# Performance work log

Hardware: AMD Instinct MI355X
Metric: run time of the kernel (lower is better)

Reference implementation:

```python
import jax, jax.numpy as jnp
import numpy as np

HIDDEN = 1024
NUM_HEADS = 16
HEAD_DIM = HIDDEN // NUM_HEADS  # 64
ROPE_DIM = HEAD_DIM // 2        # 32 (per-axis rotary dim)
EPS = 1e-6


def _make_rope_tables(dim, grid_h, grid_w, theta=10000.0):
    # pt_seq_len == ft_seq_len, so t_h = arange(H), t_w = arange(W)
    freqs = 1.0 / theta ** (np.arange(0, dim, 2, dtype=np.float32)[: dim // 2] / dim)  # [dim//2]
    fh = np.repeat(np.outer(np.arange(grid_h, dtype=np.float32), freqs), 2, axis=-1)  # [H, dim]
    fw = np.repeat(np.outer(np.arange(grid_w, dtype=np.float32), freqs), 2, axis=-1)  # [W, dim]
    fh = np.broadcast_to(fh[:, None, :], (grid_h, grid_w, dim))
    fw = np.broadcast_to(fw[None, :, :], (grid_h, grid_w, dim))
    f2d = np.concatenate([fh, fw], axis=-1).reshape(grid_h * grid_w, 2 * dim)  # [HW, 2*dim]
    return jnp.asarray(np.cos(f2d)), jnp.asarray(np.sin(f2d))


def _rms_norm(x, w, eps=EPS):
    var = jnp.mean(jnp.square(x), axis=-1, keepdims=True)
    return x * jax.lax.rsqrt(var + eps) * w


def _rotate_half(x):
    x1 = x[..., 0::2]
    x2 = x[..., 1::2]
    return jnp.stack([-x2, x1], axis=-1).reshape(x.shape)


def _apply_rope(x, cos, sin):
    # x: [B, H, S, D]; cos/sin: [S, D]
    return x * cos + _rotate_half(x) * sin


def setup_inputs() -> dict:
    key = jax.random.key(0)
    ks = jax.random.split(key, 12)
    B, IMG_H, IMG_W, CND_H, CND_W = 2, 64, 64, 32, 32
    img_len, cnd_len = IMG_H * IMG_W, CND_H * CND_W
    xav = (6.0 / (HIDDEN + HIDDEN)) ** 0.5
    inp = {
        'image_tokens': jax.random.normal(ks[0], (B, img_len, HIDDEN), jnp.float32),
        'condition_tokens': jax.random.normal(ks[1], (B, cnd_len, HIDDEN), jnp.float32),
        'q_norm_w': jnp.ones((HIDDEN,), jnp.float32),
        'kv_norm_w': jnp.ones((HIDDEN,), jnp.float32),
        'q_head_norm_w': jnp.ones((HEAD_DIM,), jnp.float32),
        'k_head_norm_w': jnp.ones((HEAD_DIM,), jnp.float32),
        'q_w': jax.random.uniform(ks[2], (HIDDEN, HIDDEN), jnp.float32, -xav, xav),
        'q_b': jnp.zeros((HIDDEN,), jnp.float32),
        'k_w': jax.random.uniform(ks[3], (HIDDEN, HIDDEN), jnp.float32, -xav, xav),
        'k_b': jnp.zeros((HIDDEN,), jnp.float32),
        'v_w': jax.random.uniform(ks[4], (HIDDEN, HIDDEN), jnp.float32, -xav, xav),
        'v_b': jnp.zeros((HIDDEN,), jnp.float32),
        'o_w': jax.random.uniform(ks[5], (HIDDEN, HIDDEN), jnp.float32, -xav, xav),
        'o_b': jnp.zeros((HIDDEN,), jnp.float32),
        'alpha': jnp.full((1,), 0.5, jnp.float32),  # nonzero so backward exercises the attn path
    }
    ic, isn = _make_rope_tables(ROPE_DIM, IMG_H, IMG_W)
    cc, cs = _make_rope_tables(ROPE_DIM, CND_H, CND_W)
    inp.update(image_cos=ic, image_sin=isn, cond_cos=cc, cond_sin=cs)
    return inp


def reference(image_tokens, condition_tokens, q_norm_w, kv_norm_w, q_head_norm_w,
              k_head_norm_w, q_w, q_b, k_w, k_b, v_w, v_b, o_w, o_b, alpha,
              image_cos, image_sin, cond_cos, cond_sin):
    B, Li, _ = image_tokens.shape
    Lc = condition_tokens.shape[1]
    qn = _rms_norm(image_tokens, q_norm_w)
    kvn = _rms_norm(condition_tokens, kv_norm_w)
    # projections (torch Linear: x @ W.T + b); weights here stored [out, in]
    q = (qn @ q_w.T + q_b).reshape(B, Li, NUM_HEADS, HEAD_DIM).transpose(0, 2, 1, 3)
    k = (kvn @ k_w.T + k_b).reshape(B, Lc, NUM_HEADS, HEAD_DIM).transpose(0, 2, 1, 3)
    v = (kvn @ v_w.T + v_b).reshape(B, Lc, NUM_HEADS, HEAD_DIM).transpose(0, 2, 1, 3)
    q = _rms_norm(q, q_head_norm_w)
    k = _rms_norm(k, k_head_norm_w)
    q = _apply_rope(q, image_cos, image_sin)
    k = _apply_rope(k, cond_cos, cond_sin)
    scale = 1.0 / jnp.sqrt(jnp.asarray(HEAD_DIM, q.dtype))
    scores = jnp.einsum('bhqd,bhkd->bhqk', q, k) * scale
    attn = jax.nn.softmax(scores, axis=-1)
    out = jnp.einsum('bhqk,bhkd->bhqd', attn, v)
    out = out.transpose(0, 2, 1, 3).reshape(B, Li, HIDDEN)
    update = out @ o_w.T + o_b
    return image_tokens + alpha.reshape(1, 1, 1) * update
```

## Files before the change

### kernel.cpp

```cpp
#include <hip/hip_runtime.h>

typedef __bf16 bf16x8 __attribute__((ext_vector_type(8)));
typedef __bf16 bf16x4 __attribute__((ext_vector_type(4)));
typedef float  f32x4  __attribute__((ext_vector_type(4)));
typedef float  f32x16 __attribute__((ext_vector_type(16)));
typedef unsigned u32x2 __attribute__((ext_vector_type(2)));

#define DEVINL __device__ __forceinline__

DEVINL void gload_lds16(const void* g, void* l) {
  __builtin_amdgcn_global_load_lds((const __attribute__((address_space(1))) void*)g,
                                   (__attribute__((address_space(3))) void*)l, 16, 0, 0);
}

DEVINL unsigned pkbf(float a, float b) {
  union { __bf16 h[2]; unsigned u; } c;
  c.h[0] = (__bf16)a; c.h[1] = (__bf16)b;
  return c.u;
}

DEVINL float fast_exp2(float x) {
#if __has_builtin(__builtin_amdgcn_exp2f)
  return __builtin_amdgcn_exp2f(x);
#else
  float r;
  asm volatile("v_exp_f32 %0, %1" : "=v"(r) : "v"(x));
  return r;
#endif
}

DEVINL float2 swap32(float x) {
  u32x2 r = __builtin_amdgcn_permlane32_swap(__float_as_uint(x), __float_as_uint(x), false, false);
  return make_float2(__uint_as_float(r.x), __uint_as_float(r.y));
}

__global__ __launch_bounds__(256) void rmsnorm2_kernel(
    const float* __restrict__ XA, const float* __restrict__ WA, __bf16* __restrict__ YA, int nA,
    const float* __restrict__ XB, const float* __restrict__ WB, __bf16* __restrict__ YB) {
  int rb = blockIdx.x, tid = threadIdx.x;
  const float* X; const float* W; __bf16* Y; int row;
  if (rb < nA) { X = XA; W = WA; Y = YA; row = rb; }
  else { X = XB; W = WB; Y = YB; row = rb - nA; }
  const float4* xr = (const float4*)(X + (size_t)row * 1024);
  float4 v = xr[tid];
  float ss = v.x * v.x + v.y * v.y + v.z * v.z + v.w * v.w;
#pragma unroll
  for (int m = 1; m < 64; m <<= 1) ss += __shfl_xor(ss, m);
  __shared__ float part[4];
  if ((tid & 63) == 0) part[tid >> 6] = ss;
  __syncthreads();
  float tot = part[0] + part[1] + part[2] + part[3];
  float rn = rsqrtf(tot * (1.0f / 1024.0f) + 1e-6f);
  float4 wv = ((const float4*)W)[tid];
  bf16x4 y;
  y[0] = (__bf16)(v.x * rn * wv.x);
  y[1] = (__bf16)(v.y * rn * wv.y);
  y[2] = (__bf16)(v.z * rn * wv.z);
  y[3] = (__bf16)(v.w * rn * wv.w);
  *(bf16x4*)(Y + (size_t)row * 1024 + tid * 4) = y;
}

__global__ __launch_bounds__(256) void cast_w_kernel(
    const float* __restrict__ a, const float* __restrict__ b,
    const float* __restrict__ c, const float* __restrict__ d,
    __bf16* __restrict__ oa, __bf16* __restrict__ ob,
    __bf16* __restrict__ oc, __bf16* __restrict__ od) {
  int gid = blockIdx.x * 256 + threadIdx.x;
  int which = gid >> 17;
  size_t off = (size_t)(gid & 131071) * 8;
  const float* s = (which == 0) ? a : (which == 1) ? b : (which == 2) ? c : d;
  __bf16* o = (which == 0) ? oa : (which == 1) ? ob : (which == 2) ? oc : od;
  float4 v0 = *(const float4*)(s + off), v1 = *(const float4*)(s + off + 4);
  bf16x8 y;
  y[0] = (__bf16)v0.x; y[1] = (__bf16)v0.y; y[2] = (__bf16)v0.z; y[3] = (__bf16)v0.w;
  y[4] = (__bf16)v1.x; y[5] = (__bf16)v1.y; y[6] = (__bf16)v1.z; y[7] = (__bf16)v1.w;
  *(bf16x8*)(o + off) = y;
}

template <int EPI>
__global__ __launch_bounds__(256) void gemm_bt_kernel(
    const __bf16* __restrict__ A, const __bf16* __restrict__ Bw,
    const float* __restrict__ bias, void* __restrict__ Cout,
    const float* __restrict__ resid, const float* __restrict__ alphap,
    const float* __restrict__ bias2, void* __restrict__ Cout2) {
  __shared__ __attribute__((aligned(16))) __bf16 As[128 * 32];
  __shared__ __attribute__((aligned(16))) __bf16 Bs[128 * 32];
  int tid = threadIdx.x, lane = tid & 63, w = tid >> 6, wr = w >> 1, wc = w & 1;
  int m0 = blockIdx.x * 128, n0 = blockIdx.y * 128;
  f32x4 z4 = {0.f, 0.f, 0.f, 0.f};
  f32x4 acc[4][4];
#pragma unroll
  for (int i = 0; i < 4; i++)
#pragma unroll
    for (int j = 0; j < 4; j++) acc[i][j] = z4;

  for (int k0 = 0; k0 < 1024; k0 += 32) {
#pragma unroll
    for (int i = 0; i < 2; i++) {
      int chunk = i * 256 + tid;
      int row = chunk >> 2, cc = chunk & 3;
      gload_lds16(A + (size_t)(m0 + row) * 1024 + k0 + cc * 8, (char*)As + i * 4096 + w * 1024);
      gload_lds16(Bw + (size_t)(n0 + row) * 1024 + k0 + cc * 8, (char*)Bs + i * 4096 + w * 1024);
    }
    __syncthreads();
    bf16x8 af[4], bfr[4];
#pragma unroll
    for (int m = 0; m < 4; m++) {
      int r = wr * 64 + m * 16 + (lane & 15);
      af[m] = *(const bf16x8*)((const char*)As + r * 64 + ((lane >> 4) << 4));
    }
#pragma unroll
    for (int n = 0; n < 4; n++) {
      int r = wc * 64 + n * 16 + (lane & 15);
      bfr[n] = *(const bf16x8*)((const char*)Bs + r * 64 + ((lane >> 4) << 4));
    }
#pragma unroll
    for (int m = 0; m < 4; m++)
#pragma unroll
      for (int n = 0; n < 4; n++)
        acc[m][n] = __builtin_amdgcn_mfma_f32_16x16x32_bf16(af[m], bfr[n], acc[m][n], 0, 0, 0);
    __syncthreads();
  }

  const float* biasU = bias;
  void* coutU = Cout;
  int nloc = n0;
  if (EPI == 2 && n0 >= 1024) { biasU = bias2; coutU = Cout2; nloc = n0 - 1024; }
  float aval = (EPI == 1) ? alphap[0] : 0.f;
#pragma unroll
  for (int m = 0; m < 4; m++)
#pragma unroll
    for (int n = 0; n < 4; n++) {
      int col = nloc + wc * 64 + n * 16 + (lane & 15);
      float bv = biasU[col];
#pragma unroll
      for (int r = 0; r < 4; r++) {
        int row = m0 + wr * 64 + m * 16 + ((lane >> 4) << 2) + r;
        size_t idx = ((size_t)row << 10) + col;
        float v = acc[m][n][r] + bv;
        if (EPI == 1)
          ((float*)coutU)[idx] = resid[idx] + aval * v;
        else
          ((__bf16*)coutU)[idx] = (__bf16)v;
      }
    }
}

__global__ __launch_bounds__(256) void headnorm_rope_kernel(
    const __bf16* __restrict__ X, const float* __restrict__ HW,
    const float* __restrict__ COS, const float* __restrict__ SIN,
    __bf16* __restrict__ Y, int log2L, float scale) {
  int tid = threadIdx.x;
  int inst = blockIdx.x * 32 + (tid >> 3);
  int sub = tid & 7;
  int token = inst >> 4, h = inst & 15;
  int L = 1 << log2L;
  int b = token >> log2L, pos = token & (L - 1);
  const __bf16* xp = X + ((size_t)token << 10) + h * 64 + sub * 8;
  bf16x8 xv = *(const bf16x8*)xp;
  float xf[8];
#pragma unroll
  for (int i = 0; i < 8; i++) xf[i] = (float)xv[i];
  float ss = 0.f;
#pragma unroll
  for (int i = 0; i < 8; i++) ss += xf[i] * xf[i];
  ss += __shfl_xor(ss, 1);
  ss += __shfl_xor(ss, 2);
  ss += __shfl_xor(ss, 4);
  float rn = rsqrtf(ss * (1.0f / 64.0f) + 1e-6f);
  const float* hwp = HW + sub * 8;
  const float* cp = COS + ((size_t)pos << 6) + sub * 8;
  const float* sp = SIN + ((size_t)pos << 6) + sub * 8;
  float xn[8], o[8];
#pragma unroll
  for (int i = 0; i < 8; i++) xn[i] = xf[i] * rn * hwp[i];
#pragma unroll
  for (int i = 0; i < 8; i += 2) {
    float c0 = cp[i], c1 = cp[i + 1], s0 = sp[i], s1 = sp[i + 1];
    o[i] = (xn[i] * c0 - xn[i + 1] * s0) * scale;
    o[i + 1] = (xn[i + 1] * c1 + xn[i] * s1) * scale;
  }
  bf16x8 yv;
#pragma unroll
  for (int i = 0; i < 8; i++) yv[i] = (__bf16)o[i];
  *(bf16x8*)(Y + (((size_t)((b << 4) + h) << log2L) + pos) * 64 + sub * 8) = yv;
}

__global__ __launch_bounds__(256) void v_transpose_kernel(
    const __bf16* __restrict__ V, __bf16* __restrict__ Vt) {
  int bx = blockIdx.x;
  int bh = bx >> 4;
  int j0 = (bx & 15) * 64;
  int b = bh >> 4, h = bh & 15;
  int tid = threadIdx.x;
#pragma unroll
  for (int it = 0; it < 2; ++it) {
    int c = it * 256 + tid;
    int jl = c >> 3, d0 = (c & 7) * 8;
    bf16x8 v = *(const bf16x8*)(V + (size_t)(b * 1024 + j0 + jl) * 1024 + h * 64 + d0);
#pragma unroll
    for (int i = 0; i < 8; i++)
      Vt[((size_t)bh * 64 + d0 + i) * 1024 + j0 + jl] = v[i];
  }
}

__global__ __launch_bounds__(256, 2) void attn_kernel(
    const __bf16* __restrict__ Qt, const float* __restrict__ QHW,
    const float* __restrict__ QCOS, const float* __restrict__ QSIN,
    const __bf16* __restrict__ Kr, const __bf16* __restrict__ Vtr,
    __bf16* __restrict__ AO) {
  int tid = threadIdx.x, lane = tid & 63, w = tid >> 6;
  int lq = lane & 31, hi = lane >> 5;
  int q0 = blockIdx.x * 256;
  int bh = blockIdx.y, b = bh >> 4, h = bh & 15;
  const float QSC = 0.125f * 1.44269504088896340736f;

  __shared__ __attribute__((aligned(16))) __bf16 Ks[2][4096];
  __shared__ __attribute__((aligned(16))) __bf16 Vs[2][4096];

  const __bf16* Kbh = Kr + ((size_t)bh << 16);
  const __bf16* Vbh = Vtr + ((size_t)bh << 16);

#pragma unroll
  for (int i = 0; i < 2; i++) {
    int s = 2 * w + i;
    int kt = s >> 2, ds = s & 3;
    gload_lds16(Kbh + (size_t)(kt * 32 + lq) * 64 + ds * 16 + hi * 8,
                (char*)Ks[0] + s * 1024);
    int f = s >> 1, dh = s & 1;
    gload_lds16(Vbh + (size_t)(dh * 32 + lq) * 1024 + f * 16 + hi * 8,
                (char*)Vs[0] + s * 1024);
  }

  bf16x8 qf[2][4];
#pragma unroll
  for (int qt = 0; qt < 2; qt++) {
    int pos = q0 + w * 64 + qt * 32 + lq;
    const __bf16* qp = Qt + ((size_t)(b * 4096 + pos) << 10) + h * 64 + hi * 8;
    float xf[4][8];
    float ss = 0.f;
#pragma unroll
    for (int ds = 0; ds < 4; ds++) {
      bf16x8 xv = *(const bf16x8*)(qp + ds * 16);
#pragma unroll
      for (int j = 0; j < 8; j++) { float f = (float)xv[j]; xf[ds][j] = f; ss += f * f; }
    }
    float2 sw = swap32(ss);
    float rn = rsqrtf((sw.x + sw.y) * (1.0f / 64.0f) + 1e-6f);
#pragma unroll
    for (int ds = 0; ds < 4; ds++) {
      int d0 = ds * 16 + hi * 8;
      const float* wp = QHW + d0;
      const float* cp = QCOS + ((size_t)pos << 6) + d0;
      const float* sp = QSIN + ((size_t)pos << 6) + d0;
      float4 wa = *(const float4*)wp, wb = *(const float4*)(wp + 4);
      float4 ca = *(const float4*)cp, cb = *(const float4*)(cp + 4);
      float4 sa = *(const float4*)sp, sb = *(const float4*)(sp + 4);
      float wv[8] = {wa.x, wa.y, wa.z, wa.w, wb.x, wb.y, wb.z, wb.w};
      float cv[8] = {ca.x, ca.y, ca.z, ca.w, cb.x, cb.y, cb.z, cb.w};
      float sv[8] = {sa.x, sa.y, sa.z, sa.w, sb.x, sb.y, sb.z, sb.w};
      float xn[8];
#pragma unroll
      for (int j = 0; j < 8; j++) xn[j] = xf[ds][j] * rn * wv[j];
      bf16x8 q8;
#pragma unroll
      for (int j = 0; j < 8; j += 2) {
        q8[j]     = (__bf16)((xn[j] * cv[j] - xn[j + 1] * sv[j]) * QSC);
        q8[j + 1] = (__bf16)((xn[j + 1] * cv[j + 1] + xn[j] * sv[j + 1]) * QSC);
      }
      qf[qt][ds] = q8;
    }
  }

  f32x16 Z16;
#pragma unroll
  for (int r = 0; r < 16; r++) Z16[r] = 0.f;

  f32x16 accO[2][2];
#pragma unroll
  for (int qt = 0; qt < 2; qt++)
#pragma unroll
    for (int dh = 0; dh < 2; dh++) accO[qt][dh] = Z16;
  float srun[2] = {0.f, 0.f};

  __syncthreads();

  int buf = 0;
  for (int t = 0; t < 16; t++) {
    if (t < 15) {
#pragma unroll
      for (int i = 0; i < 2; i++) {
        int s = 2 * w + i;
        int kt = s >> 2, ds = s & 3;
        gload_lds16(Kbh + (size_t)((t + 1) * 64 + kt * 32 + lq) * 64 + ds * 16 + hi * 8,
                    (char*)Ks[buf ^ 1] + s * 1024);
        int f = s >> 1, dh = s & 1;
        gload_lds16(Vbh + (size_t)(dh * 32 + lq) * 1024 + (t + 1) * 64 + f * 16 + hi * 8,
                    (char*)Vs[buf ^ 1] + s * 1024);
      }
    }
    const char* kbase = (const char*)Ks[buf];
    const char* vbase = (const char*)Vs[buf];
    int loff = lane * 16;

    bf16x8 kf[8], vf[8];
#pragma unroll
    for (int s = 0; s < 8; s++) kf[s] = *(const bf16x8*)(kbase + s * 1024 + loff);
#pragma unroll
    for (int s = 0; s < 8; s++) vf[s] = *(const bf16x8*)(vbase + s * 1024 + loff);

    f32x16 accS[2][2];
    __builtin_amdgcn_s_setprio(1);
#pragma unroll
    for (int qt = 0; qt < 2; qt++)
#pragma unroll
      for (int kt = 0; kt < 2; kt++) {
        accS[qt][kt] = __builtin_amdgcn_mfma_f32_32x32x16_bf16(kf[kt * 4], qf[qt][0], Z16, 0, 0, 0);
#pragma unroll
        for (int ds = 1; ds < 4; ds++)
          accS[qt][kt] = __builtin_amdgcn_mfma_f32_32x32x16_bf16(kf[kt * 4 + ds], qf[qt][ds], accS[qt][kt], 0, 0, 0);
      }
    __builtin_amdgcn_s_setprio(0);

    unsigned pa[2][4][4];
#pragma unroll
    for (int qt = 0; qt < 2; qt++) {
      float ssum = 0.f;
#pragma unroll
      for (int kt = 0; kt < 2; kt++)
#pragma unroll
        for (int r = 0; r < 16; r++) {
          float e = fast_exp2(accS[qt][kt][r]);
          accS[qt][kt][r] = e;
          ssum += e;
        }
      float2 sws = swap32(ssum);
      srun[qt] += sws.x + sws.y;
#pragma unroll
      for (int kt = 0; kt < 2; kt++)
#pragma unroll
        for (int s2 = 0; s2 < 2; s2++) {
          int f = kt * 2 + s2, rb = s2 * 8;
          unsigned u  = pkbf(accS[qt][kt][rb + 0], accS[qt][kt][rb + 1]);
          unsigned v2 = pkbf(accS[qt][kt][rb + 2], accS[qt][kt][rb + 3]);
          unsigned w2 = pkbf(accS[qt][kt][rb + 4], accS[qt][kt][rb + 5]);
          unsigned x2 = pkbf(accS[qt][kt][rb + 6], accS[qt][kt][rb + 7]);
          u32x2 r02 = __builtin_amdgcn_permlane32_swap(u, w2, false, false);
          u32x2 r13 = __builtin_amdgcn_permlane32_swap(v2, x2, false, false);
          pa[qt][f][0] = r02.x; pa[qt][f][1] = r13.x; pa[qt][f][2] = r02.y; pa[qt][f][3] = r13.y;
        }
    }

    __builtin_amdgcn_s_setprio(1);
#pragma unroll
    for (int f = 0; f < 4; f++)
#pragma unroll
      for (int qt = 0; qt < 2; qt++) {
        union { unsigned u[4]; bf16x8 v; } pf;
        pf.u[0] = pa[qt][f][0]; pf.u[1] = pa[qt][f][1];
        pf.u[2] = pa[qt][f][2]; pf.u[3] = pa[qt][f][3];
#pragma unroll
        for (int dh = 0; dh < 2; dh++)
          accO[qt][dh] = __builtin_amdgcn_mfma_f32_32x32x16_bf16(pf.v, vf[f * 2 + dh], accO[qt][dh], 0, 0, 0);
      }
    __builtin_amdgcn_s_setprio(0);
    __syncthreads();
    buf ^= 1;
  }

  __bf16* aobase = AO + (((size_t)b * 4096) << 10) + h * 64;
#pragma unroll
  for (int qt = 0; qt < 2; qt++) {
    float rinv = 1.0f / srun[qt];
    int ri = __float_as_int(rinv);
#pragma unroll
    for (int r = 0; r < 16; r++) {
      int cr = (r & 3) + ((r >> 2) << 3) + (hi << 2);
      float rv = __int_as_float(__builtin_amdgcn_ds_bpermute(cr << 2, ri));
      size_t rowoff = ((size_t)(q0 + w * 64 + qt * 32 + cr) << 10);
#pragma unroll
      for (int dh = 0; dh < 2; dh++)
        aobase[rowoff + dh * 32 + lq] = (__bf16)(accO[qt][dh][r] * rv);
    }
  }
}

extern "C" void kernel_launch(void* const* d_in, const int* in_sizes, int n_in,
                              void* d_out, int out_size, void* d_ws, size_t ws_size,
                              hipStream_t stream) {
  const float* img  = (const float*)d_in[0];
  const float* cnd  = (const float*)d_in[1];
  const float* qnw  = (const float*)d_in[2];
  const float* kvnw = (const float*)d_in[3];
  const float* qhw  = (const float*)d_in[4];
  const float* khw  = (const float*)d_in[5];
  const float* qw   = (const float*)d_in[6];
  const float* qb   = (const float*)d_in[7];
  const float* kw   = (const float*)d_in[8];
  const float* kb   = (const float*)d_in[9];
  const float* vw   = (const float*)d_in[10];
  const float* vb   = (const float*)d_in[11];
  const float* ow   = (const float*)d_in[12];
  const float* ob   = (const float*)d_in[13];
  const float* alpha= (const float*)d_in[14];
  const float* icos = (const float*)d_in[15];
  const float* isin = (const float*)d_in[16];
  const float* ccos = (const float*)d_in[17];
  const float* csin = (const float*)d_in[18];
  float* out = (float*)d_out;

  __bf16* p = (__bf16*)d_ws;
  __bf16* wqb = p; p += 1048576;
  __bf16* wkb = p; p += 1048576;
  __bf16* wvb = p; p += 1048576;
  __bf16* wob = p; p += 1048576;
  __bf16* qn  = p; p += 8388608;
  __bf16* kvn = p; p += 2097152;
  __bf16* Qt  = p; p += 8388608;
  __bf16* Kt  = p; p += 2097152;
  __bf16* Vt0 = p; p += 2097152;
  __bf16* Kr  = p; p += 2097152;
  __bf16* Vtr = p; p += 2097152;
  __bf16* AO  = qn;

  rmsnorm2_kernel<<<10240, 256, 0, stream>>>(img, qnw, qn, 8192, cnd, kvnw, kvn);
  cast_w_kernel<<<2048, 256, 0, stream>>>(qw, kw, vw, ow, wqb, wkb, wvb, wob);

  gemm_bt_kernel<0><<<dim3(64, 8), 256, 0, stream>>>(qn, wqb, qb, Qt, nullptr, nullptr, nullptr, nullptr);
  gemm_bt_kernel<2><<<dim3(16, 16), 256, 0, stream>>>(kvn, wkb, kb, Kt, nullptr, nullptr, vb, Vt0);

  headnorm_rope_kernel<<<1024, 256, 0, stream>>>(Kt, khw, ccos, csin, Kr, 10, 1.0f);
  v_transpose_kernel<<<512, 256, 0, stream>>>(Vt0, Vtr);

  attn_kernel<<<dim3(16, 32), 256, 0, stream>>>(Qt, qhw, icos, isin, Kr, Vtr, AO);

  gemm_bt_kernel<1><<<dim3(64, 8), 256, 0, stream>>>(AO, wob, ob, out, img, alpha, nullptr, nullptr);
}
```

Measured before the change: 162.1 us.

## Merge launches and triple-buffer attention K/V loads with remapped block order

```diff
diff --git a/kernel.cpp b/kernel.cpp
--- a/kernel.cpp
+++ b/kernel.cpp
@@ -34,55 +34,123 @@
   return make_float2(__uint_as_float(r.x), __uint_as_float(r.y));
 }
 
-__global__ __launch_bounds__(256) void rmsnorm2_kernel(
-    const float* __restrict__ XA, const float* __restrict__ WA, __bf16* __restrict__ YA, int nA,
-    const float* __restrict__ XB, const float* __restrict__ WB, __bf16* __restrict__ YB) {
+__global__ __launch_bounds__(256) void prep_kernel(
+    const float* __restrict__ XA, const float* __restrict__ WA, __bf16* __restrict__ YA,
+    const float* __restrict__ XB, const float* __restrict__ WB, __bf16* __restrict__ YB,
+    const float* __restrict__ wq, const float* __restrict__ wk,
+    const float* __restrict__ wv, const float* __restrict__ wo,
+    __bf16* __restrict__ oq, __bf16* __restrict__ ok,
+    __bf16* __restrict__ ov, __bf16* __restrict__ oo) {
   int rb = blockIdx.x, tid = threadIdx.x;
-  const float* X; const float* W; __bf16* Y; int row;
-  if (rb < nA) { X = XA; W = WA; Y = YA; row = rb; }
-  else { X = XB; W = WB; Y = YB; row = rb - nA; }
-  const float4* xr = (const float4*)(X + (size_t)row * 1024);
-  float4 v = xr[tid];
-  float ss = v.x * v.x + v.y * v.y + v.z * v.z + v.w * v.w;
-#pragma unroll
-  for (int m = 1; m < 64; m <<= 1) ss += __shfl_xor(ss, m);
-  __shared__ float part[4];
-  if ((tid & 63) == 0) part[tid >> 6] = ss;
-  __syncthreads();
-  float tot = part[0] + part[1] + part[2] + part[3];
-  float rn = rsqrtf(tot * (1.0f / 1024.0f) + 1e-6f);
-  float4 wv = ((const float4*)W)[tid];
-  bf16x4 y;
-  y[0] = (__bf16)(v.x * rn * wv.x);
-  y[1] = (__bf16)(v.y * rn * wv.y);
-  y[2] = (__bf16)(v.z * rn * wv.z);
-  y[3] = (__bf16)(v.w * rn * wv.w);
-  *(bf16x4*)(Y + (size_t)row * 1024 + tid * 4) = y;
-}
-
-__global__ __launch_bounds__(256) void cast_w_kernel(
-    const float* __restrict__ a, const float* __restrict__ b,
-    const float* __restrict__ c, const float* __restrict__ d,
-    __bf16* __restrict__ oa, __bf16* __restrict__ ob,
-    __bf16* __restrict__ oc, __bf16* __restrict__ od) {
-  int gid = blockIdx.x * 256 + threadIdx.x;
-  int which = gid >> 17;
-  size_t off = (size_t)(gid & 131071) * 8;
-  const float* s = (which == 0) ? a : (which == 1) ? b : (which == 2) ? c : d;
-  __bf16* o = (which == 0) ? oa : (which == 1) ? ob : (which == 2) ? oc : od;
-  float4 v0 = *(const float4*)(s + off), v1 = *(const float4*)(s + off + 4);
-  bf16x8 y;
-  y[0] = (__bf16)v0.x; y[1] = (__bf16)v0.y; y[2] = (__bf16)v0.z; y[3] = (__bf16)v0.w;
-  y[4] = (__bf16)v1.x; y[5] = (__bf16)v1.y; y[6] = (__bf16)v1.z; y[7] = (__bf16)v1.w;
-  *(bf16x8*)(o + off) = y;
-}
-
-template <int EPI>
-__global__ __launch_bounds__(256) void gemm_bt_kernel(
+  if (rb < 10240) {
+    const float* X; const float* W; __bf16* Y; int row;
+    if (rb < 8192) { X = XA; W = WA; Y = YA; row = rb; }
+    else { X = XB; W = WB; Y = YB; row = rb - 8192; }
+    const float4* xr = (const float4*)(X + (size_t)row * 1024);
+    float4 v = xr[tid];
+    float ss = v.x * v.x + v.y * v.y + v.z * v.z + v.w * v.w;
+#pragma unroll
+    for (int m = 1; m < 64; m <<= 1) ss += __shfl_xor(ss, m);
+    __shared__ float part[4];
+    if ((tid & 63) == 0) part[tid >> 6] = ss;
+    __syncthreads();
+    float tot = part[0] + part[1] + part[2] + part[3];
+    float rn = rsqrtf(tot * (1.0f / 1024.0f) + 1e-6f);
+    float4 wv4 = ((const float4*)W)[tid];
+    bf16x4 y;
+    y[0] = (__bf16)(v.x * rn * wv4.x);
+    y[1] = (__bf16)(v.y * rn * wv4.y);
+    y[2] = (__bf16)(v.z * rn * wv4.z);
+    y[3] = (__bf16)(v.w * rn * wv4.w);
+    *(bf16x4*)(Y + (size_t)row * 1024 + tid * 4) = y;
+  } else {
+    int gid = (rb - 10240) * 256 + tid;
+    int which = gid >> 17;
+    size_t off = (size_t)(gid & 131071) * 8;
+    const float* s = (which == 0) ? wq : (which == 1) ? wk : (which == 2) ? wv : wo;
+    __bf16* o = (which == 0) ? oq : (which == 1) ? ok : (which == 2) ? ov : oo;
+    float4 v0 = *(const float4*)(s + off), v1 = *(const float4*)(s + off + 4);
+    bf16x8 y;
+    y[0] = (__bf16)v0.x; y[1] = (__bf16)v0.y; y[2] = (__bf16)v0.z; y[3] = (__bf16)v0.w;
+    y[4] = (__bf16)v1.x; y[5] = (__bf16)v1.y; y[6] = (__bf16)v1.z; y[7] = (__bf16)v1.w;
+    *(bf16x8*)(o + off) = y;
+  }
+}
+
+__global__ __launch_bounds__(256) void qkv_gemm_kernel(
+    const __bf16* __restrict__ qn, const __bf16* __restrict__ kvn,
+    const __bf16* __restrict__ wq, const __bf16* __restrict__ wkv,
+    const float* __restrict__ qb, const float* __restrict__ kb, const float* __restrict__ vb,
+    __bf16* __restrict__ Qt, __bf16* __restrict__ Kt, __bf16* __restrict__ Vt0) {
+  __shared__ __attribute__((aligned(16))) __bf16 As[128 * 32];
+  __shared__ __attribute__((aligned(16))) __bf16 Bs[128 * 32];
+  int id = blockIdx.x;
+  const __bf16 *A, *Bw; const float* bias; __bf16* Cout;
+  int m0, n0, nloc;
+  if (id < 512) {
+    A = qn; Bw = wq; m0 = (id & 63) * 128; n0 = (id >> 6) * 128; nloc = n0;
+    bias = qb; Cout = Qt;
+  } else {
+    int i2 = id - 512;
+    A = kvn; Bw = wkv; m0 = (i2 & 15) * 128; n0 = (i2 >> 4) * 128;
+    if (n0 < 1024) { bias = kb; Cout = Kt; nloc = n0; }
+    else { bias = vb; Cout = Vt0; nloc = n0 - 1024; }
+  }
+  int tid = threadIdx.x, lane = tid & 63, w = tid >> 6, wr = w >> 1, wc = w & 1;
+  f32x4 z4 = {0.f, 0.f, 0.f, 0.f};
+  f32x4 acc[4][4];
+#pragma unroll
+  for (int i = 0; i < 4; i++)
+#pragma unroll
+    for (int j = 0; j < 4; j++) acc[i][j] = z4;
+
+  for (int k0 = 0; k0 < 1024; k0 += 32) {
+#pragma unroll
+    for (int i = 0; i < 2; i++) {
+      int chunk = i * 256 + tid;
+      int row = chunk >> 2, cc = chunk & 3;
+      gload_lds16(A + (size_t)(m0 + row) * 1024 + k0 + cc * 8, (char*)As + i * 4096 + w * 1024);
+      gload_lds16(Bw + (size_t)(n0 + row) * 1024 + k0 + cc * 8, (char*)Bs + i * 4096 + w * 1024);
+    }
+    __syncthreads();
+    bf16x8 af[4], bfr[4];
+#pragma unroll
+    for (int m = 0; m < 4; m++) {
+      int r = wr * 64 + m * 16 + (lane & 15);
+      af[m] = *(const bf16x8*)((const char*)As + r * 64 + ((lane >> 4) << 4));
+    }
+#pragma unroll
+    for (int n = 0; n < 4; n++) {
+      int r = wc * 64 + n * 16 + (lane & 15);
+      bfr[n] = *(const bf16x8*)((const char*)Bs + r * 64 + ((lane >> 4) << 4));
+    }
+#pragma unroll
+    for (int m = 0; m < 4; m++)
+#pragma unroll
+      for (int n = 0; n < 4; n++)
+        acc[m][n] = __builtin_amdgcn_mfma_f32_16x16x32_bf16(af[m], bfr[n], acc[m][n], 0, 0, 0);
+    __syncthreads();
+  }
+
+#pragma unroll
+  for (int m = 0; m < 4; m++)
+#pragma unroll
+    for (int n = 0; n < 4; n++) {
+      int col = nloc + wc * 64 + n * 16 + (lane & 15);
+      float bv = bias[col];
+#pragma unroll
+      for (int r = 0; r < 4; r++) {
+        int row = m0 + wr * 64 + m * 16 + ((lane >> 4) << 2) + r;
+        size_t idx = ((size_t)row << 10) + col;
+        Cout[idx] = (__bf16)(acc[m][n][r] + bv);
+      }
+    }
+}
+
+__global__ __launch_bounds__(256) void gemm_o_kernel(
     const __bf16* __restrict__ A, const __bf16* __restrict__ Bw,
-    const float* __restrict__ bias, void* __restrict__ Cout,
-    const float* __restrict__ resid, const float* __restrict__ alphap,
-    const float* __restrict__ bias2, void* __restrict__ Cout2) {
+    const float* __restrict__ bias, float* __restrict__ Cout,
+    const float* __restrict__ resid, const float* __restrict__ alphap) {
   __shared__ __attribute__((aligned(16))) __bf16 As[128 * 32];
   __shared__ __attribute__((aligned(16))) __bf16 Bs[128 * 32];
   int tid = threadIdx.x, lane = tid & 63, w = tid >> 6, wr = w >> 1, wc = w & 1;
@@ -122,85 +190,74 @@
     __syncthreads();
   }
 
-  const float* biasU = bias;
-  void* coutU = Cout;
-  int nloc = n0;
-  if (EPI == 2 && n0 >= 1024) { biasU = bias2; coutU = Cout2; nloc = n0 - 1024; }
-  float aval = (EPI == 1) ? alphap[0] : 0.f;
+  float aval = alphap[0];
 #pragma unroll
   for (int m = 0; m < 4; m++)
 #pragma unroll
     for (int n = 0; n < 4; n++) {
-      int col = nloc + wc * 64 + n * 16 + (lane & 15);
-      float bv = biasU[col];
+      int col = n0 + wc * 64 + n * 16 + (lane & 15);
+      float bv = bias[col];
 #pragma unroll
       for (int r = 0; r < 4; r++) {
         int row = m0 + wr * 64 + m * 16 + ((lane >> 4) << 2) + r;
         size_t idx = ((size_t)row << 10) + col;
-        float v = acc[m][n][r] + bv;
-        if (EPI == 1)
-          ((float*)coutU)[idx] = resid[idx] + aval * v;
-        else
-          ((__bf16*)coutU)[idx] = (__bf16)v;
+        Cout[idx] = resid[idx] + aval * (acc[m][n][r] + bv);
       }
     }
 }
 
-__global__ __launch_bounds__(256) void headnorm_rope_kernel(
-    const __bf16* __restrict__ X, const float* __restrict__ HW,
-    const float* __restrict__ COS, const float* __restrict__ SIN,
-    __bf16* __restrict__ Y, int log2L, float scale) {
-  int tid = threadIdx.x;
-  int inst = blockIdx.x * 32 + (tid >> 3);
-  int sub = tid & 7;
-  int token = inst >> 4, h = inst & 15;
-  int L = 1 << log2L;
-  int b = token >> log2L, pos = token & (L - 1);
-  const __bf16* xp = X + ((size_t)token << 10) + h * 64 + sub * 8;
-  bf16x8 xv = *(const bf16x8*)xp;
-  float xf[8];
-#pragma unroll
-  for (int i = 0; i < 8; i++) xf[i] = (float)xv[i];
-  float ss = 0.f;
-#pragma unroll
-  for (int i = 0; i < 8; i++) ss += xf[i] * xf[i];
-  ss += __shfl_xor(ss, 1);
-  ss += __shfl_xor(ss, 2);
-  ss += __shfl_xor(ss, 4);
-  float rn = rsqrtf(ss * (1.0f / 64.0f) + 1e-6f);
-  const float* hwp = HW + sub * 8;
-  const float* cp = COS + ((size_t)pos << 6) + sub * 8;
-  const float* sp = SIN + ((size_t)pos << 6) + sub * 8;
-  float xn[8], o[8];
-#pragma unroll
-  for (int i = 0; i < 8; i++) xn[i] = xf[i] * rn * hwp[i];
-#pragma unroll
-  for (int i = 0; i < 8; i += 2) {
-    float c0 = cp[i], c1 = cp[i + 1], s0 = sp[i], s1 = sp[i + 1];
-    o[i] = (xn[i] * c0 - xn[i + 1] * s0) * scale;
-    o[i + 1] = (xn[i + 1] * c1 + xn[i] * s1) * scale;
-  }
-  bf16x8 yv;
-#pragma unroll
-  for (int i = 0; i < 8; i++) yv[i] = (__bf16)o[i];
-  *(bf16x8*)(Y + (((size_t)((b << 4) + h) << log2L) + pos) * 64 + sub * 8) = yv;
-}
-
-__global__ __launch_bounds__(256) void v_transpose_kernel(
+__global__ __launch_bounds__(256) void kprep_kernel(
+    const __bf16* __restrict__ Kt, const float* __restrict__ KHW,
+    const float* __restrict__ CCOS, const float* __restrict__ CSIN,
+    __bf16* __restrict__ Kr,
     const __bf16* __restrict__ V, __bf16* __restrict__ Vt) {
-  int bx = blockIdx.x;
-  int bh = bx >> 4;
-  int j0 = (bx & 15) * 64;
-  int b = bh >> 4, h = bh & 15;
-  int tid = threadIdx.x;
-#pragma unroll
-  for (int it = 0; it < 2; ++it) {
-    int c = it * 256 + tid;
-    int jl = c >> 3, d0 = (c & 7) * 8;
-    bf16x8 v = *(const bf16x8*)(V + (size_t)(b * 1024 + j0 + jl) * 1024 + h * 64 + d0);
-#pragma unroll
-    for (int i = 0; i < 8; i++)
-      Vt[((size_t)bh * 64 + d0 + i) * 1024 + j0 + jl] = v[i];
+  int rb = blockIdx.x, tid = threadIdx.x;
+  if (rb < 1024) {
+    int inst = rb * 32 + (tid >> 3);
+    int sub = tid & 7;
+    int token = inst >> 4, h = inst & 15;
+    int b = token >> 10, pos = token & 1023;
+    const __bf16* xp = Kt + ((size_t)token << 10) + h * 64 + sub * 8;
+    bf16x8 xv = *(const bf16x8*)xp;
+    float xf[8];
+#pragma unroll
+    for (int i = 0; i < 8; i++) xf[i] = (float)xv[i];
+    float ss = 0.f;
+#pragma unroll
+    for (int i = 0; i < 8; i++) ss += xf[i] * xf[i];
+    ss += __shfl_xor(ss, 1);
+    ss += __shfl_xor(ss, 2);
+    ss += __shfl_xor(ss, 4);
+    float rn = rsqrtf(ss * (1.0f / 64.0f) + 1e-6f);
+    const float* hwp = KHW + sub * 8;
+    const float* cp = CCOS + ((size_t)pos << 6) + sub * 8;
+    const float* sp = CSIN + ((size_t)pos << 6) + sub * 8;
+    float xn[8], o[8];
+#pragma unroll
+    for (int i = 0; i < 8; i++) xn[i] = xf[i] * rn * hwp[i];
+#pragma unroll
+    for (int i = 0; i < 8; i += 2) {
+      o[i] = xn[i] * cp[i] - xn[i + 1] * sp[i];
+      o[i + 1] = xn[i + 1] * cp[i + 1] + xn[i] * sp[i + 1];
+    }
+    bf16x8 yv;
+#pragma unroll
+    for (int i = 0; i < 8; i++) yv[i] = (__bf16)o[i];
+    *(bf16x8*)(Kr + (((size_t)((b << 4) + h) << 10) + pos) * 64 + sub * 8) = yv;
+  } else {
+    int bx = rb - 1024;
+    int bh = bx >> 4;
+    int j0 = (bx & 15) * 64;
+    int b = bh >> 4, h = bh & 15;
+#pragma unroll
+    for (int it = 0; it < 2; ++it) {
+      int c = it * 256 + tid;
+      int jl = c >> 3, d0 = (c & 7) * 8;
+      bf16x8 v = *(const bf16x8*)(V + (size_t)(b * 1024 + j0 + jl) * 1024 + h * 64 + d0);
+#pragma unroll
+      for (int i = 0; i < 8; i++)
+        Vt[((size_t)bh * 64 + d0 + i) * 1024 + j0 + jl] = v[i];
+    }
   }
 }
 
@@ -211,26 +268,33 @@
     __bf16* __restrict__ AO) {
   int tid = threadIdx.x, lane = tid & 63, w = tid >> 6;
   int lq = lane & 31, hi = lane >> 5;
-  int q0 = blockIdx.x * 256;
-  int bh = blockIdx.y, b = bh >> 4, h = bh & 15;
+  int wgid = blockIdx.x;
+  int nid = (wgid & 7) * 64 + (wgid >> 3);
+  int q0 = (nid & 15) * 256;
+  int bh = nid >> 4, b = bh >> 4, h = bh & 15;
   const float QSC = 0.125f * 1.44269504088896340736f;
 
-  __shared__ __attribute__((aligned(16))) __bf16 Ks[2][4096];
-  __shared__ __attribute__((aligned(16))) __bf16 Vs[2][4096];
+  __shared__ __attribute__((aligned(16))) __bf16 Ks[3][4096];
+  __shared__ __attribute__((aligned(16))) __bf16 Vs[3][4096];
 
   const __bf16* Kbh = Kr + ((size_t)bh << 16);
   const __bf16* Vbh = Vtr + ((size_t)bh << 16);
 
-#pragma unroll
-  for (int i = 0; i < 2; i++) {
-    int s = 2 * w + i;
-    int kt = s >> 2, ds = s & 3;
-    gload_lds16(Kbh + (size_t)(kt * 32 + lq) * 64 + ds * 16 + hi * 8,
-                (char*)Ks[0] + s * 1024);
-    int f = s >> 1, dh = s & 1;
-    gload_lds16(Vbh + (size_t)(dh * 32 + lq) * 1024 + f * 16 + hi * 8,
-                (char*)Vs[0] + s * 1024);
-  }
+  auto STAGE = [&](int T, int BSEL) {
+#pragma unroll
+    for (int i = 0; i < 2; i++) {
+      int s = 2 * w + i;
+      int kt = s >> 2, ds2 = s & 3;
+      gload_lds16(Kbh + (size_t)(T * 64 + kt * 32 + lq) * 64 + ds2 * 16 + hi * 8,
+                  (char*)Ks[BSEL] + s * 1024);
+      int f = s >> 1, dh = s & 1;
+      gload_lds16(Vbh + (size_t)(dh * 32 + lq) * 1024 + T * 64 + f * 16 + hi * 8,
+                  (char*)Vs[BSEL] + s * 1024);
+    }
+  };
+
+  STAGE(0, 0);
+  STAGE(1, 1);
 
   bf16x8 qf[2][4];
 #pragma unroll
@@ -275,7 +339,6 @@
   f32x16 Z16;
 #pragma unroll
   for (int r = 0; r < 16; r++) Z16[r] = 0.f;
-
   f32x16 accO[2][2];
 #pragma unroll
   for (int qt = 0; qt < 2; qt++)
@@ -283,24 +346,15 @@
     for (int dh = 0; dh < 2; dh++) accO[qt][dh] = Z16;
   float srun[2] = {0.f, 0.f};
 
-  __syncthreads();
-
-  int buf = 0;
+  asm volatile("s_waitcnt vmcnt(4)" ::: "memory");
+  __builtin_amdgcn_s_barrier();
+  asm volatile("" ::: "memory");
+
+  int cur = 0, stg = 2;
   for (int t = 0; t < 16; t++) {
-    if (t < 15) {
-#pragma unroll
-      for (int i = 0; i < 2; i++) {
-        int s = 2 * w + i;
-        int kt = s >> 2, ds = s & 3;
-        gload_lds16(Kbh + (size_t)((t + 1) * 64 + kt * 32 + lq) * 64 + ds * 16 + hi * 8,
-                    (char*)Ks[buf ^ 1] + s * 1024);
-        int f = s >> 1, dh = s & 1;
-        gload_lds16(Vbh + (size_t)(dh * 32 + lq) * 1024 + (t + 1) * 64 + f * 16 + hi * 8,
-                    (char*)Vs[buf ^ 1] + s * 1024);
-      }
-    }
-    const char* kbase = (const char*)Ks[buf];
-    const char* vbase = (const char*)Vs[buf];
+    if (t < 14) STAGE(t + 2, stg);
+    const char* kbase = (const char*)Ks[cur];
+    const char* vbase = (const char*)Vs[cur];
     int loff = lane * 16;
 
     bf16x8 kf[8], vf[8];
@@ -364,8 +418,18 @@
           accO[qt][dh] = __builtin_amdgcn_mfma_f32_32x32x16_bf16(pf.v, vf[f * 2 + dh], accO[qt][dh], 0, 0, 0);
       }
     __builtin_amdgcn_s_setprio(0);
-    __syncthreads();
-    buf ^= 1;
+
+    if (t < 14) {
+      asm volatile("s_waitcnt vmcnt(4)" ::: "memory");
+      __builtin_amdgcn_s_barrier();
+      asm volatile("" ::: "memory");
+    } else if (t == 14) {
+      asm volatile("s_waitcnt vmcnt(0)" ::: "memory");
+      __builtin_amdgcn_s_barrier();
+      asm volatile("" ::: "memory");
+    }
+    cur = (cur == 2) ? 0 : cur + 1;
+    stg = (stg == 2) ? 0 : stg + 1;
   }
 
   __bf16* aobase = AO + (((size_t)b * 4096) << 10) + h * 64;
@@ -423,16 +487,14 @@
   __bf16* Vtr = p; p += 2097152;
   __bf16* AO  = qn;
 
-  rmsnorm2_kernel<<<10240, 256, 0, stream>>>(img, qnw, qn, 8192, cnd, kvnw, kvn);
-  cast_w_kernel<<<2048, 256, 0, stream>>>(qw, kw, vw, ow, wqb, wkb, wvb, wob);
-
-  gemm_bt_kernel<0><<<dim3(64, 8), 256, 0, stream>>>(qn, wqb, qb, Qt, nullptr, nullptr, nullptr, nullptr);
-  gemm_bt_kernel<2><<<dim3(16, 16), 256, 0, stream>>>(kvn, wkb, kb, Kt, nullptr, nullptr, vb, Vt0);
-
-  headnorm_rope_kernel<<<1024, 256, 0, stream>>>(Kt, khw, ccos, csin, Kr, 10, 1.0f);
-  v_transpose_kernel<<<512, 256, 0, stream>>>(Vt0, Vtr);
-
-  attn_kernel<<<dim3(16, 32), 256, 0, stream>>>(Qt, qhw, icos, isin, Kr, Vtr, AO);
-
-  gemm_bt_kernel<1><<<dim3(64, 8), 256, 0, stream>>>(AO, wob, ob, out, img, alpha, nullptr, nullptr);
-}
+  prep_kernel<<<12288, 256, 0, stream>>>(img, qnw, qn, cnd, kvnw, kvn,
+                                         qw, kw, vw, ow, wqb, wkb, wvb, wob);
+
+  qkv_gemm_kernel<<<768, 256, 0, stream>>>(qn, kvn, wqb, wkb, qb, kb, vb, Qt, Kt, Vt0);
+
+  kprep_kernel<<<1536, 256, 0, stream>>>(Kt, khw, ccos, csin, Kr, Vt0, Vtr);
+
+  attn_kernel<<<512, 256, 0, stream>>>(Qt, qhw, icos, isin, Kr, Vtr, AO);
+
+  gemm_o_kernel<<<dim3(64, 8), 256, 0, stream>>>(AO, wob, ob, out, img, alpha);
+}
```

Result: faster. 158.0 us (-2.5%).
